# Performance work log

Measured on AMD Instinct MI355X. Metric: run time of the kernel, lower is better.

Reference implementation:

```python
import jax, jax.numpy as jnp
import numpy as np

LAMBDA_OTDL = 1.0


def _emd2_1d(p, q):
    """Exact EMD^2 (squared-distance cost on integer grid) between two 1D
    histograms p, q of length D. For convex cost |i-j|^2 on a line the optimal
    plan is the monotone (quantile) coupling, so
      EMD2 = int_0^1 (F_p^{-1}(t) - F_q^{-1}(t))^2 dt,
    matching ot.emd2 with M[i,j] = |i-j|^2 exactly."""
    D = p.shape[0]
    cp = jnp.cumsum(p)
    cq = jnp.cumsum(q)
    t = jnp.sort(jnp.concatenate([cp, cq]))          # [2D] merged CDF breakpoints
    dt = jnp.diff(t, prepend=jnp.zeros((1,), t.dtype))
    tm = t - 0.5 * dt                                 # segment midpoints
    ip = jnp.clip(jnp.searchsorted(cp, tm, side='left'), 0, D - 1)
    iq = jnp.clip(jnp.searchsorted(cq, tm, side='left'), 0, D - 1)
    return jnp.sum(dt * (ip - iq).astype(p.dtype) ** 2)


def setup_inputs() -> dict:
    key = jax.random.key(0)
    k1, k2 = jax.random.split(key)
    B, C, D, W = 65536, 1, 256, 1
    P = jax.random.uniform(k1, (B, C, D, W), dtype=jnp.float32)
    Q = jax.random.uniform(k2, (B, C, D, W), dtype=jnp.float32)
    return {"P": P, "Q": Q}


def reference(P, Q):
    B = P.shape[0]
    P_prime = P / jnp.sum(P, axis=(2, 3), keepdims=True)
    Q_prime = Q / jnp.sum(Q, axis=(2, 3), keepdims=True)
    p_flat = P_prime.reshape(B, -1)   # [B, D] since C=W=1
    q_flat = Q_prime.reshape(B, -1)
    OT_values = jax.vmap(_emd2_1d)(p_flat, q_flat)          # [B]
    OT_values = jax.lax.stop_gradient(OT_values)            # original detaches (numpy solver)
    mse_loss = jnp.mean((P - Q) ** 2, axis=(1, 2, 3))       # [B]
    loss = mse_loss + LAMBDA_OTDL * OT_values
    return jnp.mean(loss)
```

## Files before the change

### kernel.cpp

```cpp
#include <hip/hip_runtime.h>
#include <hip/hip_fp16.h>


#define NW    4
#define DSZ   256
#define LROW  264

template <int CTRL, int RMASK, bool BC>
__device__ __forceinline__ float dpp_add(float x) {
    int t = __builtin_amdgcn_update_dpp(0, __float_as_int(x), CTRL, RMASK, 0xf, BC);
    return x + __int_as_float(t);
}

__device__ __forceinline__ float wave_scan(float x) {
    x = dpp_add<0x111, 0xf, true >(x);
    x = dpp_add<0x112, 0xf, true >(x);
    x = dpp_add<0x114, 0xf, true >(x);
    x = dpp_add<0x118, 0xf, true >(x);
    x = dpp_add<0x142, 0xa, false>(x);
    x = dpp_add<0x143, 0xc, false>(x);
    return x;
}

__device__ __forceinline__ float lane63(float x) {
    return __int_as_float(__builtin_amdgcn_readlane(__float_as_int(x), 63));
}

__device__ __forceinline__ unsigned short f2h(float x) {
    return __half_as_ushort(__float2half(x));
}
__device__ __forceinline__ float h2f(unsigned int x) {
    return __half2float(__ushort_as_half((unsigned short)x));
}

__device__ __forceinline__ float fe_stage(const float4 pv, const float4 qv,
                                          unsigned short* cp, unsigned short* cq,
                                          int lane) {
    float dx = pv.x - qv.x, dy = pv.y - qv.y;
    float dz = pv.z - qv.z, dw = pv.w - qv.w;
    float msel = dx*dx + dy*dy + dz*dz + dw*dw;

    float pl = pv.x + pv.y + pv.z + pv.w;
    float ql = qv.x + qv.y + qv.z + qv.w;
    float ps = wave_scan(pl);
    float qs = wave_scan(ql);
    float rp = __builtin_amdgcn_rcpf(lane63(ps));
    float rq = __builtin_amdgcn_rcpf(lane63(qs));
    float pe = ps - pl, qe = qs - ql;

    ushort4 hP = make_ushort4(f2h((pe + pv.x) * rp),
                              f2h((pe + pv.x + pv.y) * rp),
                              f2h((pe + pv.x + pv.y + pv.z) * rp),
                              f2h(ps * rp));
    ushort4 hQ = make_ushort4(f2h((qe + qv.x) * rq),
                              f2h((qe + qv.x + qv.y) * rq),
                              f2h((qe + qv.x + qv.y + qv.z) * rq),
                              f2h(qs * rq));
    *reinterpret_cast<ushort4*>(&cp[lane * 4]) = hP;
    *reinterpret_cast<ushort4*>(&cq[lane * 4]) = hQ;
    return msel;
}

__global__ __launch_bounds__(256, 8) void otdl_main(
    const float* __restrict__ P, const float* __restrict__ Q,
    double* __restrict__ partial, int B, int bpw)
{
    __shared__ unsigned short s_cp[NW][2][LROW];
    __shared__ unsigned short s_cq[NW][2][LROW];
    __shared__ double s_bsum[NW];

    const int tid  = threadIdx.x;
    const int wv   = tid >> 6;
    const int lane = tid & 63;
    const int wgl  = blockIdx.x * NW + wv;

    if (lane == 0) {
        s_cp[wv][0][DSZ] = 0x4000; s_cq[wv][0][DSZ] = 0x4000;
        s_cp[wv][1][DSZ] = 0x4000; s_cq[wv][1][DSZ] = 0x4000;
    }

    double acc = 0.0;
    const int  k0      = lane * 8;
    const long rowbase = (long)wgl * bpw;
    const bool is63    = (lane == 63);

    float4 pv, qv;
    {
        long c = (rowbase < B) ? rowbase : (B - 1);
        pv = reinterpret_cast<const float4*>(P + c * DSZ)[lane];
        qv = reinterpret_cast<const float4*>(Q + c * DSZ)[lane];
    }

    float mselC = fe_stage(pv, qv, s_cp[wv][0], s_cq[wv][0], lane);
    if (bpw > 1) {
        long c = (rowbase + 1 < B) ? rowbase + 1 : (B - 1);
        pv = reinterpret_cast<const float4*>(P + c * DSZ)[lane];
        qv = reinterpret_cast<const float4*>(Q + c * DSZ)[lane];
    }

#pragma unroll 2
    for (int r = 0; r < bpw; ++r) {
        const int cur = r & 1;

        float mselN = 0.0f;
        if (r + 1 < bpw) {
            mselN = fe_stage(pv, qv, s_cp[wv][cur ^ 1], s_cq[wv][cur ^ 1], lane);
        }
        if (r + 2 < bpw) {
            long c = (rowbase + r + 2 < B) ? rowbase + r + 2 : (B - 1);
            pv = reinterpret_cast<const float4*>(P + c * DSZ)[lane];
            qv = reinterpret_cast<const float4*>(Q + c * DSZ)[lane];
        }

        const unsigned short* cp = s_cp[wv][cur];
        const unsigned short* cq = s_cq[wv][cur];

        int lo = k0 > DSZ ? k0 - DSZ : 0;
        int hi = k0 < DSZ ? k0 : DSZ;
#pragma unroll
        for (int s = 0; s < 9; ++s) {
            int mid = (lo + hi) >> 1;
            int jm  = k0 - 1 - mid;
            int jr  = jm < 0 ? 0 : jm;
            unsigned int qv_ = cq[jr];
            unsigned int cv_ = cp[mid];
            bool pred = (jm < 0) || (qv_ <= cv_);
            hi = pred ? mid : hi;
            lo = pred ? lo  : mid + 1;
        }

        const unsigned short* pA = cp + lo;
        const unsigned short* pB = cq + (k0 - lo);
        float u  = (float)(4 * lo - 2 * k0 - 1);
        unsigned int a  = pA[0];
        unsigned int b2 = pB[0];
        unsigned int an = pA[1];
        unsigned int bn = pB[1];
        float e_ = 0.0f;
#pragma unroll
        for (int s = 0; s < 8; ++s) {
            bool  ea   = a < b2;
            float val  = h2f(ea ? a : b2);
            float u2   = u + 2.0f;
            float coef = ea ? -u2 : u;
            e_ = fmaf(val, coef, e_);
            u  = ea ? u2 : (u - 2.0f);
            pA += ea ? 1 : 0;
            pB += ea ? 0 : 1;
            a  = ea ? an : a;
            b2 = ea ? b2 : bn;
            an = pA[1];
            bn = pB[1];
        }

        e_ -= is63 ? fabsf(h2f(cp[DSZ - 1]) - h2f(cq[DSZ - 1])) : 0.0f;

        if (rowbase + r < B) acc += (double)(e_ + mselC * (1.0f / 256.0f));
        mselC = mselN;
    }

#pragma unroll
    for (int off = 32; off; off >>= 1) {
        double o = __shfl_xor(acc, off, 64);
        acc += o;
    }
    if (lane == 0) s_bsum[wv] = acc;
    __syncthreads();
    if (tid == 0) {
        partial[blockIdx.x] = s_bsum[0] + s_bsum[1] + s_bsum[2] + s_bsum[3];
    }
}

__global__ __launch_bounds__(256) void otdl_reduce(
    const double* __restrict__ partial, int n, float* __restrict__ out, double invB)
{
    __shared__ double sdata[256];
    double a = 0.0;
    for (int i = threadIdx.x; i < n; i += 256) a += partial[i];
    sdata[threadIdx.x] = a;
    __syncthreads();
    for (int s2 = 128; s2 > 0; s2 >>= 1) {
        if (threadIdx.x < s2) sdata[threadIdx.x] += sdata[threadIdx.x + s2];
        __syncthreads();
    }
    if (threadIdx.x == 0) out[0] = (float)(sdata[0] * invB);
}

extern "C" void kernel_launch(void* const* d_in, const int* in_sizes, int n_in,
                              void* d_out, int out_size, void* d_ws, size_t ws_size,
                              hipStream_t stream)
{
    const float* P = (const float*)d_in[0];
    const float* Q = (const float*)d_in[1];
    float* out = (float*)d_out;
    double* partial = (double*)d_ws;

    int B = in_sizes[0] / DSZ;
    const int blocks = 2048;
    const int totalWaves = blocks * NW;
    int bpw = (B + totalWaves - 1) / totalWaves;

    otdl_main<<<blocks, 256, 0, stream>>>(P, Q, partial, B, bpw);
    otdl_reduce<<<1, 256, 0, stream>>>(partial, blocks, out, 1.0 / (double)B);
}
```

Baseline: 42.34 us.

## Software-pipeline corank binary search of next row with merge of current row

The corank binary search for row r+1 is now interleaved step by step with the 8-step merge of row r, so their dependent LDS-load chains overlap instead of running one after the other. The search for the first row is peeled before the loop, and the resulting lo index is carried across iterations. On the final iteration the search reads the unused next buffer, which costs extra LDS loads but does not affect results. Register pressure rises, and the launch bounds still require 8 blocks.

```diff
diff --git a/kernel.cpp b/kernel.cpp
--- a/kernel.cpp
+++ b/kernel.cpp
@@ -61,84 +61,34 @@
     return msel;
 }
 
-__global__ __launch_bounds__(256, 8) void otdl_main(
-    const float* __restrict__ P, const float* __restrict__ Q,
-    double* __restrict__ partial, int B, int bpw)
-{
-    __shared__ unsigned short s_cp[NW][2][LROW];
-    __shared__ unsigned short s_cq[NW][2][LROW];
-    __shared__ double s_bsum[NW];
-
-    const int tid  = threadIdx.x;
-    const int wv   = tid >> 6;
-    const int lane = tid & 63;
-    const int wgl  = blockIdx.x * NW + wv;
-
-    if (lane == 0) {
-        s_cp[wv][0][DSZ] = 0x4000; s_cq[wv][0][DSZ] = 0x4000;
-        s_cp[wv][1][DSZ] = 0x4000; s_cq[wv][1][DSZ] = 0x4000;
-    }
-
-    double acc = 0.0;
-    const int  k0      = lane * 8;
-    const long rowbase = (long)wgl * bpw;
-    const bool is63    = (lane == 63);
-
-    float4 pv, qv;
-    {
-        long c = (rowbase < B) ? rowbase : (B - 1);
-        pv = reinterpret_cast<const float4*>(P + c * DSZ)[lane];
-        qv = reinterpret_cast<const float4*>(Q + c * DSZ)[lane];
-    }
-
-    float mselC = fe_stage(pv, qv, s_cp[wv][0], s_cq[wv][0], lane);
-    if (bpw > 1) {
-        long c = (rowbase + 1 < B) ? rowbase + 1 : (B - 1);
-        pv = reinterpret_cast<const float4*>(P + c * DSZ)[lane];
-        qv = reinterpret_cast<const float4*>(Q + c * DSZ)[lane];
-    }
-
-#pragma unroll 2
-    for (int r = 0; r < bpw; ++r) {
-        const int cur = r & 1;
-
-        float mselN = 0.0f;
-        if (r + 1 < bpw) {
-            mselN = fe_stage(pv, qv, s_cp[wv][cur ^ 1], s_cq[wv][cur ^ 1], lane);
-        }
-        if (r + 2 < bpw) {
-            long c = (rowbase + r + 2 < B) ? rowbase + r + 2 : (B - 1);
-            pv = reinterpret_cast<const float4*>(P + c * DSZ)[lane];
-            qv = reinterpret_cast<const float4*>(Q + c * DSZ)[lane];
-        }
-
-        const unsigned short* cp = s_cp[wv][cur];
-        const unsigned short* cq = s_cq[wv][cur];
-
-        int lo = k0 > DSZ ? k0 - DSZ : 0;
-        int hi = k0 < DSZ ? k0 : DSZ;
+__device__ __forceinline__ float corank_merge(
+    const unsigned short* cpN, const unsigned short* cqN,
+    const unsigned short* cpC, const unsigned short* cqC,
+    int k0, int loC, bool is63, int& loN)
+{
+    int lo = k0 > DSZ ? k0 - DSZ : 0;
+    int hi = k0 < DSZ ? k0 : DSZ;
+    const unsigned short* pA = cpC + loC;
+    const unsigned short* pB = cqC + (k0 - loC);
+    float u  = (float)(4 * loC - 2 * k0 - 1);
+    unsigned int a  = pA[0];
+    unsigned int b2 = pB[0];
+    unsigned int an = pA[1];
+    unsigned int bn = pB[1];
+    float e_ = 0.0f;
 #pragma unroll
-        for (int s = 0; s < 9; ++s) {
+    for (int s = 0; s < 9; ++s) {
+        {
             int mid = (lo + hi) >> 1;
             int jm  = k0 - 1 - mid;
             int jr  = jm < 0 ? 0 : jm;
-            unsigned int qv_ = cq[jr];
-            unsigned int cv_ = cp[mid];
-            bool pred = (jm < 0) || (qv_ <= cv_);
+            unsigned int qq = cqN[jr];
+            unsigned int cc = cpN[mid];
+            bool pred = (jm < 0) || (qq <= cc);
             hi = pred ? mid : hi;
             lo = pred ? lo  : mid + 1;
         }
-
-        const unsigned short* pA = cp + lo;
-        const unsigned short* pB = cq + (k0 - lo);
-        float u  = (float)(4 * lo - 2 * k0 - 1);
-        unsigned int a  = pA[0];
-        unsigned int b2 = pB[0];
-        unsigned int an = pA[1];
-        unsigned int bn = pB[1];
-        float e_ = 0.0f;
-#pragma unroll
-        for (int s = 0; s < 8; ++s) {
+        if (s < 8) {
             bool  ea   = a < b2;
             float val  = h2f(ea ? a : b2);
             float u2   = u + 2.0f;
@@ -152,11 +102,92 @@
             an = pA[1];
             bn = pB[1];
         }
-
-        e_ -= is63 ? fabsf(h2f(cp[DSZ - 1]) - h2f(cq[DSZ - 1])) : 0.0f;
+    }
+    loN = lo;
+    e_ -= is63 ? fabsf(h2f(cpC[DSZ - 1]) - h2f(cqC[DSZ - 1])) : 0.0f;
+    return e_;
+}
+
+__global__ __launch_bounds__(256, 8) void otdl_main(
+    const float* __restrict__ P, const float* __restrict__ Q,
+    double* __restrict__ partial, int B, int bpw)
+{
+    __shared__ unsigned short s_cp[NW][2][LROW];
+    __shared__ unsigned short s_cq[NW][2][LROW];
+    __shared__ double s_bsum[NW];
+
+    const int tid  = threadIdx.x;
+    const int wv   = tid >> 6;
+    const int lane = tid & 63;
+    const int wgl  = blockIdx.x * NW + wv;
+
+    if (lane == 0) {
+        s_cp[wv][0][DSZ] = 0x4000; s_cq[wv][0][DSZ] = 0x4000;
+        s_cp[wv][1][DSZ] = 0x4000; s_cq[wv][1][DSZ] = 0x4000;
+    }
+
+    double acc = 0.0;
+    const int  k0      = lane * 8;
+    const long rowbase = (long)wgl * bpw;
+    const bool is63    = (lane == 63);
+
+    float4 pv, qv;
+    {
+        long c = (rowbase < B) ? rowbase : (B - 1);
+        pv = reinterpret_cast<const float4*>(P + c * DSZ)[lane];
+        qv = reinterpret_cast<const float4*>(Q + c * DSZ)[lane];
+    }
+
+    float mselC = fe_stage(pv, qv, s_cp[wv][0], s_cq[wv][0], lane);
+    if (bpw > 1) {
+        long c = (rowbase + 1 < B) ? rowbase + 1 : (B - 1);
+        pv = reinterpret_cast<const float4*>(P + c * DSZ)[lane];
+        qv = reinterpret_cast<const float4*>(Q + c * DSZ)[lane];
+    }
+    int loC;
+    {
+        const unsigned short* cp = s_cp[wv][0];
+        const unsigned short* cq = s_cq[wv][0];
+        int lo = k0 > DSZ ? k0 - DSZ : 0;
+        int hi = k0 < DSZ ? k0 : DSZ;
+#pragma unroll
+        for (int s = 0; s < 9; ++s) {
+            int mid = (lo + hi) >> 1;
+            int jm  = k0 - 1 - mid;
+            int jr  = jm < 0 ? 0 : jm;
+            unsigned int qq = cq[jr];
+            unsigned int cc = cp[mid];
+            bool pred = (jm < 0) || (qq <= cc);
+            hi = pred ? mid : hi;
+            lo = pred ? lo  : mid + 1;
+        }
+        loC = lo;
+    }
+
+#pragma unroll 2
+    for (int r = 0; r < bpw; ++r) {
+        const int cur = r & 1;
+        unsigned short* cpN = s_cp[wv][cur ^ 1];
+        unsigned short* cqN = s_cq[wv][cur ^ 1];
+        const unsigned short* cpC = s_cp[wv][cur];
+        const unsigned short* cqC = s_cq[wv][cur];
+
+        float mselN = 0.0f;
+        if (r + 1 < bpw) {
+            mselN = fe_stage(pv, qv, cpN, cqN, lane);
+        }
+        if (r + 2 < bpw) {
+            long c = (rowbase + r + 2 < B) ? rowbase + r + 2 : (B - 1);
+            pv = reinterpret_cast<const float4*>(P + c * DSZ)[lane];
+            qv = reinterpret_cast<const float4*>(Q + c * DSZ)[lane];
+        }
+
+        int loN;
+        float e_ = corank_merge(cpN, cqN, cpC, cqC, k0, loC, is63, loN);
 
         if (rowbase + r < B) acc += (double)(e_ + mselC * (1.0f / 256.0f));
         mselC = mselN;
+        loC   = loN;
     }
 
 #pragma unroll
```

Result: no change. 42.91 us (+1.4%).

## Process two rows per wave using half-wave scans and 16-step merges

Applied to the files above, without the earlier changes.

Each wave now handles two rows at once, one per 32-lane half. Each lane loads 8 elements per row, scans with a 32-lane DPP scan, and merges 16 steps per lane instead of 8. This halves the number of serial per-row iterations and the wave-wide scan depth per row, and packs the fp16 CDF stores into 128-bit writes. In exchange it raises register and LDS use, so the occupancy hint drops from 8 to 6. The pair tail needs care: the row index is clamped and accumulation is guarded, and this assumes rows per wave fit the pairing.

```diff
diff --git a/kernel.cpp b/kernel.cpp
--- a/kernel.cpp
+++ b/kernel.cpp
@@ -12,108 +12,142 @@
     return x + __int_as_float(t);
 }
 
-__device__ __forceinline__ float wave_scan(float x) {
+__device__ __forceinline__ float half_scan(float x) {
     x = dpp_add<0x111, 0xf, true >(x);
     x = dpp_add<0x112, 0xf, true >(x);
     x = dpp_add<0x114, 0xf, true >(x);
     x = dpp_add<0x118, 0xf, true >(x);
     x = dpp_add<0x142, 0xa, false>(x);
-    x = dpp_add<0x143, 0xc, false>(x);
     return x;
 }
 
-__device__ __forceinline__ float lane63(float x) {
+__device__ __forceinline__ float rdlane31(float x) {
+    return __int_as_float(__builtin_amdgcn_readlane(__float_as_int(x), 31));
+}
+__device__ __forceinline__ float rdlane63(float x) {
     return __int_as_float(__builtin_amdgcn_readlane(__float_as_int(x), 63));
 }
 
-__device__ __forceinline__ unsigned short f2h(float x) {
-    return __half_as_ushort(__float2half(x));
+__device__ __forceinline__ unsigned int f2h(float x) {
+    return (unsigned int)__half_as_ushort(__float2half(x));
 }
 __device__ __forceinline__ float h2f(unsigned int x) {
     return __half2float(__ushort_as_half((unsigned short)x));
 }
 
-__device__ __forceinline__ float fe_stage(const float4 pv, const float4 qv,
-                                          unsigned short* cp, unsigned short* cq,
-                                          int lane) {
-    float dx = pv.x - qv.x, dy = pv.y - qv.y;
-    float dz = pv.z - qv.z, dw = pv.w - qv.w;
-    float msel = dx*dx + dy*dy + dz*dz + dw*dw;
-
-    float pl = pv.x + pv.y + pv.z + pv.w;
-    float ql = qv.x + qv.y + qv.z + qv.w;
-    float ps = wave_scan(pl);
-    float qs = wave_scan(ql);
-    float rp = __builtin_amdgcn_rcpf(lane63(ps));
-    float rq = __builtin_amdgcn_rcpf(lane63(qs));
+__device__ __forceinline__ float fe_stage(
+    const float4 pA, const float4 pB, const float4 qA, const float4 qB,
+    unsigned short* cp, unsigned short* cq, int l32, bool hiHalf)
+{
+    float d0 = pA.x - qA.x, d1 = pA.y - qA.y, d2 = pA.z - qA.z, d3 = pA.w - qA.w;
+    float d4 = pB.x - qB.x, d5 = pB.y - qB.y, d6 = pB.z - qB.z, d7 = pB.w - qB.w;
+    float msel = d0*d0 + d1*d1 + d2*d2 + d3*d3 + d4*d4 + d5*d5 + d6*d6 + d7*d7;
+
+    float pl = (pA.x + pA.y + pA.z + pA.w) + (pB.x + pB.y + pB.z + pB.w);
+    float ql = (qA.x + qA.y + qA.z + qA.w) + (qB.x + qB.y + qB.z + qB.w);
+    float ps = half_scan(pl);
+    float qs = half_scan(ql);
+
+    float ptot = hiHalf ? rdlane63(ps) : rdlane31(ps);
+    float qtot = hiHalf ? rdlane63(qs) : rdlane31(qs);
+    float rp = __builtin_amdgcn_rcpf(ptot);
+    float rq = __builtin_amdgcn_rcpf(qtot);
     float pe = ps - pl, qe = qs - ql;
 
-    ushort4 hP = make_ushort4(f2h((pe + pv.x) * rp),
-                              f2h((pe + pv.x + pv.y) * rp),
-                              f2h((pe + pv.x + pv.y + pv.z) * rp),
-                              f2h(ps * rp));
-    ushort4 hQ = make_ushort4(f2h((qe + qv.x) * rq),
-                              f2h((qe + qv.x + qv.y) * rq),
-                              f2h((qe + qv.x + qv.y + qv.z) * rq),
-                              f2h(qs * rq));
-    *reinterpret_cast<ushort4*>(&cp[lane * 4]) = hP;
-    *reinterpret_cast<ushort4*>(&cq[lane * 4]) = hQ;
+    float p0 = pe + pA.x, p1 = p0 + pA.y, p2 = p1 + pA.z, p3 = p2 + pA.w;
+    float p4 = p3 + pB.x, p5 = p4 + pB.y, p6 = p5 + pB.z;
+    float q0 = qe + qA.x, q1 = q0 + qA.y, q2 = q1 + qA.z, q3 = q2 + qA.w;
+    float q4 = q3 + qB.x, q5 = q4 + qB.y, q6 = q5 + qB.z;
+
+    uint4 wp, wq;
+    wp.x = f2h(p0 * rp) | (f2h(p1 * rp) << 16);
+    wp.y = f2h(p2 * rp) | (f2h(p3 * rp) << 16);
+    wp.z = f2h(p4 * rp) | (f2h(p5 * rp) << 16);
+    wp.w = f2h(p6 * rp) | (f2h(ps * rp) << 16);
+    wq.x = f2h(q0 * rq) | (f2h(q1 * rq) << 16);
+    wq.y = f2h(q2 * rq) | (f2h(q3 * rq) << 16);
+    wq.z = f2h(q4 * rq) | (f2h(q5 * rq) << 16);
+    wq.w = f2h(q6 * rq) | (f2h(qs * rq) << 16);
+
+    *reinterpret_cast<uint4*>(&cp[l32 * 8]) = wp;
+    *reinterpret_cast<uint4*>(&cq[l32 * 8]) = wq;
     return msel;
 }
 
-__global__ __launch_bounds__(256, 8) void otdl_main(
+__global__ __launch_bounds__(256, 6) void otdl_main(
     const float* __restrict__ P, const float* __restrict__ Q,
     double* __restrict__ partial, int B, int bpw)
 {
-    __shared__ unsigned short s_cp[NW][2][LROW];
-    __shared__ unsigned short s_cq[NW][2][LROW];
+    __shared__ unsigned short s_cp[NW][2][2][LROW];
+    __shared__ unsigned short s_cq[NW][2][2][LROW];
     __shared__ double s_bsum[NW];
 
     const int tid  = threadIdx.x;
     const int wv   = tid >> 6;
     const int lane = tid & 63;
+    const int l32  = lane & 31;
+    const bool hiHalf = (lane >= 32);
+    const int rh   = hiHalf ? 1 : 0;
     const int wgl  = blockIdx.x * NW + wv;
 
     if (lane == 0) {
-        s_cp[wv][0][DSZ] = 0x4000; s_cq[wv][0][DSZ] = 0x4000;
-        s_cp[wv][1][DSZ] = 0x4000; s_cq[wv][1][DSZ] = 0x4000;
+#pragma unroll
+        for (int bf = 0; bf < 2; ++bf)
+#pragma unroll
+            for (int r2 = 0; r2 < 2; ++r2) {
+                s_cp[wv][bf][r2][DSZ] = 0x4000;
+                s_cq[wv][bf][r2][DSZ] = 0x4000;
+            }
     }
 
     double acc = 0.0;
-    const int  k0      = lane * 8;
+    const int  k0      = l32 * 16;
+    const int  npair   = (bpw + 1) >> 1;
     const long rowbase = (long)wgl * bpw;
-    const bool is63    = (lane == 63);
-
-    float4 pv, qv;
+    const bool isLast  = (l32 == 31);
+
+    float4 pA, pB, qA, qB;
     {
-        long c = (rowbase < B) ? rowbase : (B - 1);
-        pv = reinterpret_cast<const float4*>(P + c * DSZ)[lane];
-        qv = reinterpret_cast<const float4*>(Q + c * DSZ)[lane];
-    }
-
-    float mselC = fe_stage(pv, qv, s_cp[wv][0], s_cq[wv][0], lane);
-    if (bpw > 1) {
-        long c = (rowbase + 1 < B) ? rowbase + 1 : (B - 1);
-        pv = reinterpret_cast<const float4*>(P + c * DSZ)[lane];
-        qv = reinterpret_cast<const float4*>(Q + c * DSZ)[lane];
+        long b = rowbase + rh;
+        long c = (b < B) ? b : (B - 1);
+        const float4* Pr = reinterpret_cast<const float4*>(P + c * DSZ + l32 * 8);
+        const float4* Qr = reinterpret_cast<const float4*>(Q + c * DSZ + l32 * 8);
+        pA = Pr[0]; pB = Pr[1];
+        qA = Qr[0]; qB = Qr[1];
+    }
+
+    float mselC = fe_stage(pA, pB, qA, qB, s_cp[wv][0][rh], s_cq[wv][0][rh],
+                           l32, hiHalf);
+    if (npair > 1) {
+        long b = rowbase + 2 + rh;
+        long c = (b < B) ? b : (B - 1);
+        const float4* Pr = reinterpret_cast<const float4*>(P + c * DSZ + l32 * 8);
+        const float4* Qr = reinterpret_cast<const float4*>(Q + c * DSZ + l32 * 8);
+        pA = Pr[0]; pB = Pr[1];
+        qA = Qr[0]; qB = Qr[1];
     }
 
 #pragma unroll 2
-    for (int r = 0; r < bpw; ++r) {
-        const int cur = r & 1;
+    for (int p = 0; p < npair; ++p) {
+        const int cur = p & 1;
 
         float mselN = 0.0f;
-        if (r + 1 < bpw) {
-            mselN = fe_stage(pv, qv, s_cp[wv][cur ^ 1], s_cq[wv][cur ^ 1], lane);
-        }
-        if (r + 2 < bpw) {
-            long c = (rowbase + r + 2 < B) ? rowbase + r + 2 : (B - 1);
-            pv = reinterpret_cast<const float4*>(P + c * DSZ)[lane];
-            qv = reinterpret_cast<const float4*>(Q + c * DSZ)[lane];
-        }
-
-        const unsigned short* cp = s_cp[wv][cur];
-        const unsigned short* cq = s_cq[wv][cur];
+        if (p + 1 < npair) {
+            mselN = fe_stage(pA, pB, qA, qB,
+                             s_cp[wv][cur ^ 1][rh], s_cq[wv][cur ^ 1][rh],
+                             l32, hiHalf);
+        }
+        if (p + 2 < npair) {
+            long b = rowbase + 2 * (p + 2) + rh;
+            long c = (b < B) ? b : (B - 1);
+            const float4* Pr = reinterpret_cast<const float4*>(P + c * DSZ + l32 * 8);
+            const float4* Qr = reinterpret_cast<const float4*>(Q + c * DSZ + l32 * 8);
+            pA = Pr[0]; pB = Pr[1];
+            qA = Qr[0]; qB = Qr[1];
+        }
+
+        const unsigned short* cp = s_cp[wv][cur][rh];
+        const unsigned short* cq = s_cq[wv][cur][rh];
 
         int lo = k0 > DSZ ? k0 - DSZ : 0;
         int hi = k0 < DSZ ? k0 : DSZ;
@@ -122,40 +156,41 @@
             int mid = (lo + hi) >> 1;
             int jm  = k0 - 1 - mid;
             int jr  = jm < 0 ? 0 : jm;
-            unsigned int qv_ = cq[jr];
-            unsigned int cv_ = cp[mid];
-            bool pred = (jm < 0) || (qv_ <= cv_);
+            unsigned int qq = cq[jr];
+            unsigned int cc = cp[mid];
+            bool pred = (jm < 0) || (qq <= cc);
             hi = pred ? mid : hi;
             lo = pred ? lo  : mid + 1;
         }
 
-        const unsigned short* pA = cp + lo;
-        const unsigned short* pB = cq + (k0 - lo);
+        const unsigned short* pA_ = cp + lo;
+        const unsigned short* pB_ = cq + (k0 - lo);
         float u  = (float)(4 * lo - 2 * k0 - 1);
-        unsigned int a  = pA[0];
-        unsigned int b2 = pB[0];
-        unsigned int an = pA[1];
-        unsigned int bn = pB[1];
+        unsigned int a  = pA_[0];
+        unsigned int b2 = pB_[0];
+        unsigned int an = pA_[1];
+        unsigned int bn = pB_[1];
         float e_ = 0.0f;
 #pragma unroll
-        for (int s = 0; s < 8; ++s) {
+        for (int s = 0; s < 16; ++s) {
             bool  ea   = a < b2;
             float val  = h2f(ea ? a : b2);
             float u2   = u + 2.0f;
             float coef = ea ? -u2 : u;
             e_ = fmaf(val, coef, e_);
             u  = ea ? u2 : (u - 2.0f);
-            pA += ea ? 1 : 0;
-            pB += ea ? 0 : 1;
+            pA_ += ea ? 1 : 0;
+            pB_ += ea ? 0 : 1;
             a  = ea ? an : a;
             b2 = ea ? b2 : bn;
-            an = pA[1];
-            bn = pB[1];
-        }
-
-        e_ -= is63 ? fabsf(h2f(cp[DSZ - 1]) - h2f(cq[DSZ - 1])) : 0.0f;
-
-        if (rowbase + r < B) acc += (double)(e_ + mselC * (1.0f / 256.0f));
+            an = pA_[1];
+            bn = pB_[1];
+        }
+
+        e_ -= isLast ? fabsf(h2f(cp[DSZ - 1]) - h2f(cq[DSZ - 1])) : 0.0f;
+
+        if (rowbase + 2 * p + rh < B)
+            acc += (double)(e_ + mselC * (1.0f / 256.0f));
         mselC = mselN;
     }
 
```

New measurement: 38.97 us. 8.0% less time.
